# Performance work log

Hardware: AMD Instinct MI355X
Metric: run time of the kernel (lower is better)

Reference implementation:

```python
import jax, jax.numpy as jnp
import numpy as np

NUM_LAYERS, B, S, H = 2, 32, 4096, 1024
NEG_INF = -1.0e9


def setup_inputs() -> dict:
    key = jax.random.key(0)
    k1, k2, k3 = jax.random.split(key, 3)
    hidden = jax.random.normal(k1, (NUM_LAYERS, B, H), dtype=jnp.float32)
    encoder_outputs = jax.random.normal(k2, (B, S, H), dtype=jnp.float32)
    mask = jax.random.randint(k3, (B, S), 0, 2).astype(jnp.bool_)
    return {"hidden": hidden, "encoder_outputs": encoder_outputs, "mask": mask}


def reference(hidden, encoder_outputs, mask):
    # hidden: [L, B, H] -> take last layer [B, H]
    h = hidden[-1]
    # scores: [B, S] = einsum over H
    scores = jnp.einsum("bsh,bh->bs", encoder_outputs, h)
    scores = jnp.where(mask, scores, NEG_INF)
    attn = jax.nn.softmax(scores, axis=1)  # [B, S]
    # context: [B, H]
    context = jnp.einsum("bs,bsh->bh", attn, encoder_outputs)
    return (context, attn)
```

## Files before the change

kernel.cpp:

```cpp
#include <hip/hip_runtime.h>
#include <math.h>

#define B_ 32
#define S_ 4096
#define H_ 1024
#define NBLK 32
#define ROWS_PER_BLOCK (S_ / NBLK)
#define NWAVE 4
#define ROWS_PER_WAVE (ROWS_PER_BLOCK / NWAVE)
#define CHUNK 4
#define NCHUNK (ROWS_PER_WAVE / CHUNK)
#define NEG_INF_ -1.0e9f

__global__ __launch_bounds__(256, 4) void attn_pass1(
    const float* __restrict__ hidden,
    const float* __restrict__ enc,
    const int*   __restrict__ mask,
    float* __restrict__ scores,
    float* __restrict__ part_ctx,
    float* __restrict__ part_ml)
{
    const int blk  = blockIdx.x;
    const int b    = blk >> 5;
    const int cb   = blk & 31;
    const int tid  = threadIdx.x;
    const int wave = tid >> 6;
    const int lane = tid & 63;

    const float4* h4 = (const float4*)(hidden + (size_t)(B_ + b) * H_);
    const float4 hf0 = h4[lane];
    const float4 hf1 = h4[lane + 64];
    const float4 hf2 = h4[lane + 128];
    const float4 hf3 = h4[lane + 192];

    float m = -INFINITY;
    float l = 0.0f;
    float4 c0 = {0.f, 0.f, 0.f, 0.f};
    float4 c1 = c0, c2 = c0, c3 = c0;
    float myscore = 0.0f;

    const int    row0  = cb * ROWS_PER_BLOCK + wave * ROWS_PER_WAVE;
    const float* encb  = enc  + (size_t)b * S_ * H_;
    const int*   maskb = mask + (size_t)b * S_;

    for (int k = 0; k < NCHUNK; ++k) {
        const int sbase = row0 + k * CHUNK;

        float4 r[CHUNK][4];
        #pragma unroll
        for (int c = 0; c < CHUNK; ++c) {
            const float4* row4 = (const float4*)(encb + (size_t)(sbase + c) * H_);
            r[c][0] = row4[lane];
            r[c][1] = row4[lane + 64];
            r[c][2] = row4[lane + 128];
            r[c][3] = row4[lane + 192];
        }

        float pd[CHUNK];
        #pragma unroll
        for (int c = 0; c < CHUNK; ++c) {
            float d = r[c][0].x * hf0.x + r[c][0].y * hf0.y + r[c][0].z * hf0.z + r[c][0].w * hf0.w;
            d += r[c][1].x * hf1.x + r[c][1].y * hf1.y + r[c][1].z * hf1.z + r[c][1].w * hf1.w;
            d += r[c][2].x * hf2.x + r[c][2].y * hf2.y + r[c][2].z * hf2.z + r[c][2].w * hf2.w;
            d += r[c][3].x * hf3.x + r[c][3].y * hf3.y + r[c][3].z * hf3.z + r[c][3].w * hf3.w;
            pd[c] = d;
        }

        #pragma unroll
        for (int off = 32; off >= 1; off >>= 1) {
            #pragma unroll
            for (int c = 0; c < CHUNK; ++c)
                pd[c] += __shfl_xor(pd[c], off, 64);
        }

        float sc[CHUNK];
        #pragma unroll
        for (int c = 0; c < CHUNK; ++c) {
            sc[c] = (maskb[sbase + c] != 0) ? pd[c] : NEG_INF_;
            if (lane == k * CHUNK + c) myscore = sc[c];
        }

        float cmax = fmaxf(fmaxf(sc[0], sc[1]), fmaxf(sc[2], sc[3]));
        const float newm  = fmaxf(m, cmax);
        const float scale = __expf(m - newm);
        float p[CHUNK];
        float psum = 0.0f;
        #pragma unroll
        for (int c = 0; c < CHUNK; ++c) { p[c] = __expf(sc[c] - newm); psum += p[c]; }
        l = l * scale + psum;

        c0.x *= scale; c0.y *= scale; c0.z *= scale; c0.w *= scale;
        c1.x *= scale; c1.y *= scale; c1.z *= scale; c1.w *= scale;
        c2.x *= scale; c2.y *= scale; c2.z *= scale; c2.w *= scale;
        c3.x *= scale; c3.y *= scale; c3.z *= scale; c3.w *= scale;
        #pragma unroll
        for (int c = 0; c < CHUNK; ++c) {
            c0.x += p[c] * r[c][0].x;  c0.y += p[c] * r[c][0].y;
            c0.z += p[c] * r[c][0].z;  c0.w += p[c] * r[c][0].w;
            c1.x += p[c] * r[c][1].x;  c1.y += p[c] * r[c][1].y;
            c1.z += p[c] * r[c][1].z;  c1.w += p[c] * r[c][1].w;
            c2.x += p[c] * r[c][2].x;  c2.y += p[c] * r[c][2].y;
            c2.z += p[c] * r[c][2].z;  c2.w += p[c] * r[c][2].w;
            c3.x += p[c] * r[c][3].x;  c3.y += p[c] * r[c][3].y;
            c3.z += p[c] * r[c][3].z;  c3.w += p[c] * r[c][3].w;
        }
        m = newm;
    }

    if (lane < ROWS_PER_WAVE)
        scores[(size_t)b * S_ + row0 + lane] = myscore;

    __shared__ float lds_ctx[NWAVE][H_];
    __shared__ float lds_m[NWAVE];
    __shared__ float lds_l[NWAVE];
    float4* dst = (float4*)lds_ctx[wave];
    dst[lane]       = c0;
    dst[lane + 64]  = c1;
    dst[lane + 128] = c2;
    dst[lane + 192] = c3;
    if (lane == 0) { lds_m[wave] = m; lds_l[wave] = l; }
    __syncthreads();

    const float M  = fmaxf(fmaxf(lds_m[0], lds_m[1]), fmaxf(lds_m[2], lds_m[3]));
    const float w0 = __expf(lds_m[0] - M);
    const float w1 = __expf(lds_m[1] - M);
    const float w2 = __expf(lds_m[2] - M);
    const float w3 = __expf(lds_m[3] - M);

    const int e = tid * 4;
    const float4 a0 = *(const float4*)&lds_ctx[0][e];
    const float4 a1 = *(const float4*)&lds_ctx[1][e];
    const float4 a2 = *(const float4*)&lds_ctx[2][e];
    const float4 a3 = *(const float4*)&lds_ctx[3][e];
    float4 o;
    o.x = a0.x * w0 + a1.x * w1 + a2.x * w2 + a3.x * w3;
    o.y = a0.y * w0 + a1.y * w1 + a2.y * w2 + a3.y * w3;
    o.z = a0.z * w0 + a1.z * w1 + a2.z * w2 + a3.z * w3;
    o.w = a0.w * w0 + a1.w * w1 + a2.w * w2 + a3.w * w3;
    *(float4*)&part_ctx[(size_t)blk * H_ + e] = o;

    if (tid == 0) {
        const float L = lds_l[0] * w0 + lds_l[1] * w1 + lds_l[2] * w2 + lds_l[3] * w3;
        part_ml[blk * 2]     = M;
        part_ml[blk * 2 + 1] = L;
    }
}

__global__ __launch_bounds__(256) void attn_pass2(
    const float* __restrict__ part_ctx,
    const float* __restrict__ part_ml,
    float* __restrict__ out_ctx,
    float* __restrict__ attn)
{
    const int b    = blockIdx.x;
    const int part = blockIdx.y;
    const int tid  = threadIdx.x;

    float M = -INFINITY;
    #pragma unroll
    for (int p = 0; p < NBLK; ++p)
        M = fmaxf(M, part_ml[(b * NBLK + p) * 2]);

    float L = 0.0f;
    float w[NBLK];
    #pragma unroll
    for (int p = 0; p < NBLK; ++p) {
        w[p] = __expf(part_ml[(b * NBLK + p) * 2] - M);
        L += part_ml[(b * NBLK + p) * 2 + 1] * w[p];
    }
    const float invL = 1.0f / L;

    if (part == 0) {
        const int e = tid * 4;
        float4 acc = {0.f, 0.f, 0.f, 0.f};
        #pragma unroll
        for (int p = 0; p < NBLK; ++p) {
            const float4 v = *(const float4*)&part_ctx[(size_t)(b * NBLK + p) * H_ + e];
            acc.x += v.x * w[p];  acc.y += v.y * w[p];
            acc.z += v.z * w[p];  acc.w += v.w * w[p];
        }
        acc.x *= invL; acc.y *= invL; acc.z *= invL; acc.w *= invL;
        *(float4*)&out_ctx[(size_t)b * H_ + e] = acc;
    } else {
        const size_t s0 = (size_t)b * S_ + (size_t)(part - 1) * 1024 + tid * 4;
        float4 sc = *(const float4*)&attn[s0];
        sc.x = __expf(sc.x - M) * invL;
        sc.y = __expf(sc.y - M) * invL;
        sc.z = __expf(sc.z - M) * invL;
        sc.w = __expf(sc.w - M) * invL;
        *(float4*)&attn[s0] = sc;
    }
}

extern "C" void kernel_launch(void* const* d_in, const int* in_sizes, int n_in,
                              void* d_out, int out_size, void* d_ws, size_t ws_size,
                              hipStream_t stream) {
    (void)in_sizes; (void)n_in; (void)out_size; (void)ws_size;
    const float* hidden = (const float*)d_in[0];
    const float* enc    = (const float*)d_in[1];
    const int*   mask   = (const int*)d_in[2];

    float* out      = (float*)d_out;
    float* out_ctx  = out;
    float* attn     = out + (size_t)B_ * H_;

    float* part_ctx = (float*)d_ws;
    float* part_ml  = part_ctx + (size_t)B_ * NBLK * H_;

    attn_pass1<<<dim3(B_ * NBLK), dim3(256), 0, stream>>>(
        hidden, enc, mask, attn, part_ctx, part_ml);
    attn_pass2<<<dim3(B_, 5), dim3(256), 0, stream>>>(
        part_ctx, part_ml, out_ctx, attn);
}
```

Baseline: 693.2 us.

## Double-buffer encoder row loads with nontemporal reads and ballot-precomputed mask

Restructures the pass-1 streaming loop into a software-pipelined double buffer. The next chunk of encoder rows is loaded, with nontemporal hints, while the current chunk is reduced, and the chunk size drops from 4 to 2 rows to keep register use in check. Per-row mask loads are replaced by a single coalesced load plus a wave ballot bitmask. Arithmetic is rewritten with ext_vector_type vectors. The fully unrolled loop and the double buffer raise register pressure, which could lower occupancy at launch_bounds(256,4).

```diff
diff --git a/kernel.cpp b/kernel.cpp
--- a/kernel.cpp
+++ b/kernel.cpp
@@ -1,5 +1,7 @@
 #include <hip/hip_runtime.h>
 #include <math.h>
+
+typedef float v4f __attribute__((ext_vector_type(4)));
 
 #define B_ 32
 #define S_ 4096
@@ -8,7 +10,7 @@
 #define ROWS_PER_BLOCK (S_ / NBLK)
 #define NWAVE 4
 #define ROWS_PER_WAVE (ROWS_PER_BLOCK / NWAVE)
-#define CHUNK 4
+#define CHUNK 2
 #define NCHUNK (ROWS_PER_WAVE / CHUNK)
 #define NEG_INF_ -1.0e9f
 
@@ -27,43 +29,53 @@
     const int wave = tid >> 6;
     const int lane = tid & 63;
 
-    const float4* h4 = (const float4*)(hidden + (size_t)(B_ + b) * H_);
-    const float4 hf0 = h4[lane];
-    const float4 hf1 = h4[lane + 64];
-    const float4 hf2 = h4[lane + 128];
-    const float4 hf3 = h4[lane + 192];
-
-    float m = -INFINITY;
-    float l = 0.0f;
-    float4 c0 = {0.f, 0.f, 0.f, 0.f};
-    float4 c1 = c0, c2 = c0, c3 = c0;
-    float myscore = 0.0f;
+    const v4f* h4 = (const v4f*)(hidden + (size_t)(B_ + b) * H_);
+    const v4f hf0 = h4[lane];
+    const v4f hf1 = h4[lane + 64];
+    const v4f hf2 = h4[lane + 128];
+    const v4f hf3 = h4[lane + 192];
 
     const int    row0  = cb * ROWS_PER_BLOCK + wave * ROWS_PER_WAVE;
     const float* encb  = enc  + (size_t)b * S_ * H_;
     const int*   maskb = mask + (size_t)b * S_;
 
+    const int mval = (lane < ROWS_PER_WAVE) ? maskb[row0 + lane] : 0;
+    const unsigned long long mbits = __ballot(mval != 0);
+
+    float m = -INFINITY;
+    float l = 0.0f;
+    v4f c0 = (v4f)0.0f, c1 = (v4f)0.0f, c2 = (v4f)0.0f, c3 = (v4f)0.0f;
+    float myscore = 0.0f;
+
+    v4f buf[2][CHUNK][4];
+
+    auto load_chunk = [&](int k, int slot) {
+        #pragma unroll
+        for (int c = 0; c < CHUNK; ++c) {
+            const v4f* row4 = (const v4f*)(encb + (size_t)(row0 + k * CHUNK + c) * H_);
+            buf[slot][c][0] = __builtin_nontemporal_load(&row4[lane]);
+            buf[slot][c][1] = __builtin_nontemporal_load(&row4[lane + 64]);
+            buf[slot][c][2] = __builtin_nontemporal_load(&row4[lane + 128]);
+            buf[slot][c][3] = __builtin_nontemporal_load(&row4[lane + 192]);
+        }
+    };
+
+    load_chunk(0, 0);
+
+    #pragma unroll
     for (int k = 0; k < NCHUNK; ++k) {
-        const int sbase = row0 + k * CHUNK;
-
-        float4 r[CHUNK][4];
+        const int cur = k & 1;
+        if (k + 1 < NCHUNK) load_chunk(k + 1, cur ^ 1);
+
+        float pd[CHUNK];
         #pragma unroll
         for (int c = 0; c < CHUNK; ++c) {
-            const float4* row4 = (const float4*)(encb + (size_t)(sbase + c) * H_);
-            r[c][0] = row4[lane];
-            r[c][1] = row4[lane + 64];
-            r[c][2] = row4[lane + 128];
-            r[c][3] = row4[lane + 192];
-        }
-
-        float pd[CHUNK];
-        #pragma unroll
-        for (int c = 0; c < CHUNK; ++c) {
-            float d = r[c][0].x * hf0.x + r[c][0].y * hf0.y + r[c][0].z * hf0.z + r[c][0].w * hf0.w;
-            d += r[c][1].x * hf1.x + r[c][1].y * hf1.y + r[c][1].z * hf1.z + r[c][1].w * hf1.w;
-            d += r[c][2].x * hf2.x + r[c][2].y * hf2.y + r[c][2].z * hf2.z + r[c][2].w * hf2.w;
-            d += r[c][3].x * hf3.x + r[c][3].y * hf3.y + r[c][3].z * hf3.z + r[c][3].w * hf3.w;
-            pd[c] = d;
+            const v4f p0 = buf[cur][c][0] * hf0;
+            const v4f p1 = buf[cur][c][1] * hf1;
+            const v4f p2 = buf[cur][c][2] * hf2;
+            const v4f p3 = buf[cur][c][3] * hf3;
+            const v4f ps = p0 + p1 + p2 + p3;
+            pd[c] = ps.x + ps.y + ps.z + ps.w;
         }
 
         #pragma unroll
@@ -76,48 +88,35 @@
         float sc[CHUNK];
         #pragma unroll
         for (int c = 0; c < CHUNK; ++c) {
-            sc[c] = (maskb[sbase + c] != 0) ? pd[c] : NEG_INF_;
+            sc[c] = ((mbits >> (k * CHUNK + c)) & 1ULL) ? pd[c] : NEG_INF_;
             if (lane == k * CHUNK + c) myscore = sc[c];
         }
 
-        float cmax = fmaxf(fmaxf(sc[0], sc[1]), fmaxf(sc[2], sc[3]));
+        const float cmax  = fmaxf(sc[0], sc[1]);
         const float newm  = fmaxf(m, cmax);
         const float scale = __expf(m - newm);
         float p[CHUNK];
-        float psum = 0.0f;
-        #pragma unroll
-        for (int c = 0; c < CHUNK; ++c) { p[c] = __expf(sc[c] - newm); psum += p[c]; }
-        l = l * scale + psum;
-
-        c0.x *= scale; c0.y *= scale; c0.z *= scale; c0.w *= scale;
-        c1.x *= scale; c1.y *= scale; c1.z *= scale; c1.w *= scale;
-        c2.x *= scale; c2.y *= scale; c2.z *= scale; c2.w *= scale;
-        c3.x *= scale; c3.y *= scale; c3.z *= scale; c3.w *= scale;
-        #pragma unroll
-        for (int c = 0; c < CHUNK; ++c) {
-            c0.x += p[c] * r[c][0].x;  c0.y += p[c] * r[c][0].y;
-            c0.z += p[c] * r[c][0].z;  c0.w += p[c] * r[c][0].w;
-            c1.x += p[c] * r[c][1].x;  c1.y += p[c] * r[c][1].y;
-            c1.z += p[c] * r[c][1].z;  c1.w += p[c] * r[c][1].w;
-            c2.x += p[c] * r[c][2].x;  c2.y += p[c] * r[c][2].y;
-            c2.z += p[c] * r[c][2].z;  c2.w += p[c] * r[c][2].w;
-            c3.x += p[c] * r[c][3].x;  c3.y += p[c] * r[c][3].y;
-            c3.z += p[c] * r[c][3].z;  c3.w += p[c] * r[c][3].w;
-        }
+        #pragma unroll
+        for (int c = 0; c < CHUNK; ++c) p[c] = __expf(sc[c] - newm);
+        l = l * scale + p[0] + p[1];
+
+        c0 = c0 * scale + p[0] * buf[cur][0][0] + p[1] * buf[cur][1][0];
+        c1 = c1 * scale + p[0] * buf[cur][0][1] + p[1] * buf[cur][1][1];
+        c2 = c2 * scale + p[0] * buf[cur][0][2] + p[1] * buf[cur][1][2];
+        c3 = c3 * scale + p[0] * buf[cur][0][3] + p[1] * buf[cur][1][3];
         m = newm;
     }
 
     if (lane < ROWS_PER_WAVE)
         scores[(size_t)b * S_ + row0 + lane] = myscore;
 
-    __shared__ float lds_ctx[NWAVE][H_];
+    __shared__ v4f lds_ctx[NWAVE][H_ / 4];
     __shared__ float lds_m[NWAVE];
     __shared__ float lds_l[NWAVE];
-    float4* dst = (float4*)lds_ctx[wave];
-    dst[lane]       = c0;
-    dst[lane + 64]  = c1;
-    dst[lane + 128] = c2;
-    dst[lane + 192] = c3;
+    lds_ctx[wave][lane]       = c0;
+    lds_ctx[wave][lane + 64]  = c1;
+    lds_ctx[wave][lane + 128] = c2;
+    lds_ctx[wave][lane + 192] = c3;
     if (lane == 0) { lds_m[wave] = m; lds_l[wave] = l; }
     __syncthreads();
 
@@ -127,17 +126,9 @@
     const float w2 = __expf(lds_m[2] - M);
     const float w3 = __expf(lds_m[3] - M);
 
-    const int e = tid * 4;
-    const float4 a0 = *(const float4*)&lds_ctx[0][e];
-    const float4 a1 = *(const float4*)&lds_ctx[1][e];
-    const float4 a2 = *(const float4*)&lds_ctx[2][e];
-    const float4 a3 = *(const float4*)&lds_ctx[3][e];
-    float4 o;
-    o.x = a0.x * w0 + a1.x * w1 + a2.x * w2 + a3.x * w3;
-    o.y = a0.y * w0 + a1.y * w1 + a2.y * w2 + a3.y * w3;
-    o.z = a0.z * w0 + a1.z * w1 + a2.z * w2 + a3.z * w3;
-    o.w = a0.w * w0 + a1.w * w1 + a2.w * w2 + a3.w * w3;
-    *(float4*)&part_ctx[(size_t)blk * H_ + e] = o;
+    const v4f o = lds_ctx[0][tid] * w0 + lds_ctx[1][tid] * w1 +
+                  lds_ctx[2][tid] * w2 + lds_ctx[3][tid] * w3;
+    *(v4f*)&part_ctx[(size_t)blk * H_ + tid * 4] = o;
 
     if (tid == 0) {
         const float L = lds_l[0] * w0 + lds_l[1] * w1 + lds_l[2] * w2 + lds_l[3] * w3;
@@ -172,23 +163,22 @@
 
     if (part == 0) {
         const int e = tid * 4;
-        float4 acc = {0.f, 0.f, 0.f, 0.f};
+        v4f acc = (v4f)0.0f;
         #pragma unroll
         for (int p = 0; p < NBLK; ++p) {
-            const float4 v = *(const float4*)&part_ctx[(size_t)(b * NBLK + p) * H_ + e];
-            acc.x += v.x * w[p];  acc.y += v.y * w[p];
-            acc.z += v.z * w[p];  acc.w += v.w * w[p];
-        }
-        acc.x *= invL; acc.y *= invL; acc.z *= invL; acc.w *= invL;
-        *(float4*)&out_ctx[(size_t)b * H_ + e] = acc;
+            const v4f v = *(const v4f*)&part_ctx[(size_t)(b * NBLK + p) * H_ + e];
+            acc += v * w[p];
+        }
+        acc *= invL;
+        *(v4f*)&out_ctx[(size_t)b * H_ + e] = acc;
     } else {
         const size_t s0 = (size_t)b * S_ + (size_t)(part - 1) * 1024 + tid * 4;
-        float4 sc = *(const float4*)&attn[s0];
+        v4f sc = *(const v4f*)&attn[s0];
         sc.x = __expf(sc.x - M) * invL;
         sc.y = __expf(sc.y - M) * invL;
         sc.z = __expf(sc.z - M) * invL;
         sc.w = __expf(sc.w - M) * invL;
-        *(float4*)&attn[s0] = sc;
+        *(v4f*)&attn[s0] = sc;
     }
 }
 
```

Result: slower. 882.7 us (+27.3%).
